# Optimization experiments

Hardware: AMD Instinct MI355X
Metric: run time of the kernel (lower is better)

The kernel has to match this reference:

```python
import jax, jax.numpy as jnp
import numpy as np

A = 20000        # distinct library arcs
T = 500000       # timing arcs in design
S = 8            # LUT slew-axis length
C = 8            # LUT load-axis length
G = 250000       # gates
TOTAL_U = 1000000  # gate x candidate-master entries
SCALE = 1.0e15
MAX_CAP = 1.0e-12
MAX_ITER = 3


def _axis_interval(ax, x):
    """ax: [M,K] monotone axes, x: [M]. Returns lower index i0 in [0,K-2] and frac a (may extrapolate)."""
    K = ax.shape[1]
    i0 = jnp.clip(jnp.sum(ax <= x[:, None], axis=1) - 1, 0, K - 2)
    ar = jnp.arange(ax.shape[0])
    x0 = ax[ar, i0]
    x1 = ax[ar, i0 + 1]
    a = (x - x0) / (x1 - x0)
    return i0, a


def _bilinear_gate(in_slew, load, dtab, stab, axs, axc):
    """Batched bilinear interpolation into per-arc 2D LUTs. All leading dims M."""
    M = in_slew.shape[0]
    ar = jnp.arange(M)
    i0, a = _axis_interval(axs, in_slew)
    j0, b = _axis_interval(axc, load)
    i1, j1 = i0 + 1, j0 + 1

    def _blerp(t):
        return ((1 - a) * (1 - b) * t[ar, i0, j0]
                + (1 - a) * b * t[ar, i0, j1]
                + a * (1 - b) * t[ar, i1, j0]
                + a * b * t[ar, i1, j1])

    return _blerp(dtab), _blerp(stab)


def _compute_ceff_batch(in_slew, c1, c2, rpi, dtab, stab, axs, axc, max_iter=MAX_ITER):
    ceff = jnp.maximum(c1 + c2, 1e-30)
    for _ in range(max_iter):
        d, _ = _bilinear_gate(in_slew, ceff, dtab, stab, axs, axc)
        tau = jnp.maximum(d, 1e-30)
        ratio = jnp.minimum(2.0 * tau / jnp.maximum(in_slew, 1e-30), 10.0)
        h = jnp.where(ratio > 0.01, (1.0 - jnp.exp(-ratio)) / ratio, 1.0 - ratio / 2.0)
        ceff = jnp.maximum(c1 + c2 * h, 1e-30)
    return ceff


def _segment_softmax(logits, gate_id, num_groups):
    """Numerically stable per-gate softmax via segment reductions."""
    gmax = jax.ops.segment_max(logits, gate_id, num_segments=num_groups)
    ex = jnp.exp(logits - gmax[gate_id])
    gsum = jax.ops.segment_sum(ex, gate_id, num_segments=num_groups)
    return ex / gsum[gate_id]


def _gate_grouped_forward(in_arr, in_slew, c1, c2, rpi, arc_idx_r, arc_idx_f,
                          unateness, delay_table, slew_table, load_index, slew_index):
    t = arc_idx_r.shape[0]
    arc_flat = jnp.stack([arc_idx_r, arc_idx_f], axis=1).reshape(-1)  # [2T]
    una = unateness[arc_flat]
    is_fall = jnp.arange(2 * t, dtype=una.dtype) % 2
    rf_idx = (una ^ is_fall).reshape(t, 2)  # rise/fall select per column
    in_slew_sel = jnp.take_along_axis(in_slew, rf_idx, axis=1).reshape(-1)
    in_arr_sel = jnp.take_along_axis(in_arr, rf_idx, axis=1).reshape(-1)

    dtab = delay_table[arc_flat]   # [2T,S,C] big gather (memory bound)
    stab = slew_table[arc_flat]
    axc = load_index[arc_flat]     # [2T,C]
    axs = slew_index[arc_flat]     # [2T,S]

    c1_f = jnp.repeat(c1, 2) / SCALE
    c2_f = jnp.repeat(c2, 2) / SCALE
    rpi_f = jnp.repeat(rpi, 2)
    load = _compute_ceff_batch(in_slew_sel, c1_f, c2_f, rpi_f, dtab, stab, axs, axc)
    load = jnp.minimum(load, MAX_CAP)

    arc_delay, arc_slew = _bilinear_gate(in_slew_sel, load, dtab, stab, axs, axc)
    arr_out = (in_arr_sel + arc_delay).reshape(t, 2)
    slew_out = arc_slew.reshape(t, 2)
    return jnp.concatenate([arr_out, slew_out], axis=1)  # [T,4]


def setup_inputs() -> dict:
    key = jax.random.key(0)
    ks = jax.random.split(key, 14)
    U_flat = jax.random.normal(ks[0], (TOTAL_U,), jnp.float32)
    gate_id = jnp.sort(jax.random.randint(ks[1], (TOTAL_U,), 0, G, dtype=jnp.int32))
    in_arr = jax.random.normal(ks[2], (T, 2), jnp.float32)
    in_slew = jax.random.uniform(ks[3], (T, 2), jnp.float32, 0.05, 3.0)
    c1 = jax.random.uniform(ks[4], (T,), jnp.float32, 0.0, 1.0)
    c2 = jax.random.uniform(ks[5], (T,), jnp.float32, 0.0, 1.0)
    rpi = jax.random.uniform(ks[6], (T,), jnp.float32, 0.1, 1.0)
    arc_idx_r = jax.random.randint(ks[7], (T,), 0, A, dtype=jnp.int32)
    arc_idx_f = jax.random.randint(ks[8], (T,), 0, A, dtype=jnp.int32)
    unateness = jax.random.randint(ks[9], (A,), 0, 2, dtype=jnp.int32)
    delay_table = jax.random.uniform(ks[10], (A, S, C), jnp.float32, 0.01, 1.0)
    slew_table = jax.random.uniform(ks[11], (A, S, C), jnp.float32, 0.01, 1.0)
    # strictly increasing LUT axes: slew axis ~[0.05, 4], load axis ~[5e-17, 3e-15]
    slew_index = jnp.cumsum(jax.random.uniform(ks[12], (A, S), jnp.float32, 0.05, 0.6), axis=1)
    load_index = jnp.cumsum(jax.random.uniform(ks[13], (A, C), jnp.float32, 0.05, 0.6), axis=1) * 1e-15
    return dict(U_flat=U_flat, gate_id=gate_id, in_arr=in_arr, in_slew=in_slew,
                c1=c1, c2=c2, rpi=rpi, arc_idx_r=arc_idx_r, arc_idx_f=arc_idx_f,
                unateness=unateness, delay_table=delay_table, slew_table=slew_table,
                slew_index=slew_index, load_index=load_index)


def reference(U_flat, gate_id, in_arr, in_slew, c1, c2, rpi, arc_idx_r, arc_idx_f,
              unateness, delay_table, slew_table, slew_index, load_index):
    weights = _segment_softmax(U_flat, gate_id, G)  # per-gate soft master selection
    out = _gate_grouped_forward(in_arr, in_slew, c1, c2, rpi, arc_idx_r, arc_idx_f,
                                unateness, delay_table, slew_table, load_index, slew_index)
    return out, weights
```

## Files before the change

kernel.cpp:

```cpp
#include <hip/hip_runtime.h>

#define T_N 500000
#define U_N 1000000
#define A_N 20000

#define SBLK 256
#define HALO 96

#define TIMING_BLOCKS ((T_N + 255) / 256)
#define SOFTMAX_BLOCKS ((U_N + SBLK - 1) / SBLK)

typedef float vfloat2 __attribute__((ext_vector_type(2)));
typedef float vfloat4 __attribute__((ext_vector_type(4)));
typedef float vfloat8 __attribute__((ext_vector_type(8)));

__device__ __forceinline__ float sel8(vfloat8 r, int j) {
    float v = r[0];
    v = (j >= 1) ? r[1] : v;
    v = (j >= 2) ? r[2] : v;
    v = (j >= 3) ? r[3] : v;
    v = (j >= 4) ? r[4] : v;
    v = (j >= 5) ? r[5] : v;
    v = (j >= 6) ? r[6] : v;
    v = (j >= 7) ? r[7] : v;
    return v;
}

__device__ __forceinline__ vfloat8 load8v(const float* __restrict__ p) {
    return *(const vfloat8*)p;
}


__global__ void __launch_bounds__(256, 1)
fused_kernel(
             const float2* __restrict__ in_arr,
             const float2* __restrict__ in_slew,
             const float* __restrict__ c1,
             const float* __restrict__ c2,
             const int* __restrict__ arc_r,
             const int* __restrict__ arc_f,
             const int* __restrict__ una,
             const float* __restrict__ dtab,
             const float* __restrict__ stab,
             const float* __restrict__ sidx,
             const float* __restrict__ lidx,
             float4* __restrict__ out,
             const float* __restrict__ U,
             const int* __restrict__ gid,
             float* __restrict__ wout)
{
    __shared__ float se[SBLK + 2 * HALO];
    __shared__ int   sg[SBLK + 2 * HALO];

    if (blockIdx.x >= TIMING_BLOCKS) {
        int sblk = blockIdx.x - TIMING_BLOCKS;
        int base = sblk * SBLK;
        int wstart = base - HALO;

        for (int k = threadIdx.x; k < SBLK + 2 * HALO; k += SBLK) {
            int idx = wstart + k;
            if (idx >= 0 && idx < U_N) {
                se[k] = expf(__builtin_nontemporal_load(U + idx));
                sg[k] = __builtin_nontemporal_load(gid + idx);
            } else {
                se[k] = 0.0f;
                sg[k] = -1 - k;
            }
        }
        __syncthreads();

        int i = base + threadIdx.x;
        if (i >= U_N) return;

        int li = threadIdx.x + HALO;
        int g = sg[li];
        float mye = se[li];
        float s = mye;
        for (int j = li - 1; j >= 0 && sg[j] == g; --j) s += se[j];
        for (int j = li + 1; j < SBLK + 2 * HALO && sg[j] == g; ++j) s += se[j];

        __builtin_nontemporal_store(mye / s, wout + i);
        return;
    }

    int t = blockIdx.x * blockDim.x + threadIdx.x;
    if (t >= T_N) return;

    vfloat2 ia = __builtin_nontemporal_load((const vfloat2*)in_arr + t);
    vfloat2 is = __builtin_nontemporal_load((const vfloat2*)in_slew + t);
    float c1f = __builtin_nontemporal_load(c1 + t) / 1.0e15f;
    float c2f = __builtin_nontemporal_load(c2 + t) / 1.0e15f;
    int arcs0 = __builtin_nontemporal_load(arc_r + t);
    int arcs1 = __builtin_nontemporal_load(arc_f + t);

    float res_arr[2], res_slew[2];

#pragma unroll
    for (int col = 0; col < 2; ++col) {
        int arc = (col == 0) ? arcs0 : arcs1;
        int u   = una[arc];
        int rf  = u ^ col;
        float slew = rf ? is.y : is.x;
        float arr  = rf ? ia.y : ia.x;

        vfloat8 s  = load8v(sidx + (size_t)arc * 8);
        vfloat8 cx = load8v(lidx + (size_t)arc * 8);

        int cnt = 0;
#pragma unroll
        for (int k = 0; k < 8; ++k) cnt += (s[k] <= slew) ? 1 : 0;
        int i0 = min(max(cnt - 1, 0), 6);
        float x0 = sel8(s, i0);
        float x1 = sel8(s, i0 + 1);
        float a = (slew - x0) / (x1 - x0);
        float om_a = 1.0f - a;

        vfloat8 d0 = load8v(dtab + (size_t)arc * 64 + (size_t)i0 * 8);
        vfloat8 d1 = load8v(dtab + (size_t)arc * 64 + (size_t)i0 * 8 + 8);

        float slew_den = fmaxf(slew, 1e-30f);
        float ceff = fmaxf(c1f + c2f, 1e-30f);
#pragma unroll
        for (int it = 0; it < 3; ++it) {
            int jc = 0;
#pragma unroll
            for (int k = 0; k < 8; ++k) jc += (cx[k] <= ceff) ? 1 : 0;
            int j0 = min(max(jc - 1, 0), 6);
            float y0 = sel8(cx, j0);
            float y1 = sel8(cx, j0 + 1);
            float b = (ceff - y0) / (y1 - y0);
            float om_b = 1.0f - b;
            float v00 = sel8(d0, j0), v01 = sel8(d0, j0 + 1);
            float v10 = sel8(d1, j0), v11 = sel8(d1, j0 + 1);
            float d = om_a * om_b * v00 + om_a * b * v01
                    + a * om_b * v10 + a * b * v11;
            float tau = fmaxf(d, 1e-30f);
            float ratio = fminf(2.0f * tau / slew_den, 10.0f);
            float h = (ratio > 0.01f) ? (1.0f - expf(-ratio)) / ratio
                                      : 1.0f - 0.5f * ratio;
            ceff = fmaxf(c1f + c2f * h, 1e-30f);
        }
        float load = fminf(ceff, 1.0e-12f);

        int jc = 0;
#pragma unroll
        for (int k = 0; k < 8; ++k) jc += (cx[k] <= load) ? 1 : 0;
        int j0 = min(max(jc - 1, 0), 6);
        float y0 = sel8(cx, j0);
        float y1 = sel8(cx, j0 + 1);
        float b = (load - y0) / (y1 - y0);
        float om_b = 1.0f - b;

        float v00 = sel8(d0, j0), v01 = sel8(d0, j0 + 1);
        float v10 = sel8(d1, j0), v11 = sel8(d1, j0 + 1);
        float delay = om_a * om_b * v00 + om_a * b * v01
                    + a * om_b * v10 + a * b * v11;

        const float* srow = stab + (size_t)arc * 64 + (size_t)i0 * 8;
        float s00 = srow[j0],     s01 = srow[j0 + 1];
        float s10 = srow[8 + j0], s11 = srow[8 + j0 + 1];
        float sl = om_a * om_b * s00 + om_a * b * s01
                 + a * om_b * s10 + a * b * s11;

        res_arr[col]  = arr + delay;
        res_slew[col] = sl;
    }

    vfloat4 o = {res_arr[0], res_arr[1], res_slew[0], res_slew[1]};
    __builtin_nontemporal_store(o, (vfloat4*)out + t);
}

extern "C" void kernel_launch(void* const* d_in, const int* in_sizes, int n_in,
                              void* d_out, int out_size, void* d_ws, size_t ws_size,
                              hipStream_t stream) {
    const float*  U      = (const float*)d_in[0];
    const int*    gid    = (const int*)d_in[1];
    const float2* in_arr = (const float2*)d_in[2];
    const float2* in_slw = (const float2*)d_in[3];
    const float*  c1     = (const float*)d_in[4];
    const float*  c2     = (const float*)d_in[5];
    const int*    arc_r  = (const int*)d_in[7];
    const int*    arc_f  = (const int*)d_in[8];
    const int*    una    = (const int*)d_in[9];
    const float*  dtab   = (const float*)d_in[10];
    const float*  stab   = (const float*)d_in[11];
    const float*  sidx   = (const float*)d_in[12];
    const float*  lidx   = (const float*)d_in[13];

    float* out  = (float*)d_out;
    float* wout = out + (size_t)T_N * 4;

    fused_kernel<<<TIMING_BLOCKS + SOFTMAX_BLOCKS, 256, 0, stream>>>(
        in_arr, in_slw, c1, c2, arc_r, arc_f, una, dtab, stab, sidx, lidx,
        (float4*)out, U, gid, wout);
}
```

Baseline: 144.9 us.

## Repack LUT axes and tables into interleaved workspace layout, bit-pack unateness into LDS

A pre-pass kernel interleaves the slew and load axes per arc, interleaves the delay and slew tables row by row, and packs unateness into a bitmask. The main kernel loads that bitmask into shared memory per timing block and reads the interleaved layouts, so each random arc gather touches fewer cache lines. The cost is an extra launch plus about 11 MB of repacking traffic on every call, and a per-block LDS fill of 625 words. A fallback path keeps the original kernel when the workspace is too small.

```diff
diff --git a/kernel.cpp b/kernel.cpp
--- a/kernel.cpp
+++ b/kernel.cpp
@@ -9,6 +9,13 @@
 
 #define TIMING_BLOCKS ((T_N + 255) / 256)
 #define SOFTMAX_BLOCKS ((U_N + SBLK - 1) / SBLK)
+
+#define UNA_WORDS ((A_N + 31) / 32)
+#define META_BYTES (A_N * 16 * 4)
+#define UNA_BYTES  (UNA_WORDS * 4)
+#define PK_BYTES   (A_N * 128 * 4)
+#define WS_META    (META_BYTES + UNA_BYTES)
+#define WS_FULL    (META_BYTES + UNA_BYTES + PK_BYTES)
 
 typedef float vfloat2 __attribute__((ext_vector_type(2)));
 typedef float vfloat4 __attribute__((ext_vector_type(4)));
@@ -31,26 +38,60 @@
 }
 
 
+__global__ void __launch_bounds__(256)
+repack_kernel(const float* __restrict__ sidx, const float* __restrict__ lidx,
+              const float* __restrict__ dtab, const float* __restrict__ stab,
+              const int* __restrict__ una,
+              float* __restrict__ meta, unsigned* __restrict__ una_pk,
+              float* __restrict__ pk, int do_tables)
+{
+    int gtid = blockIdx.x * 256 + threadIdx.x;
+    int gs   = gridDim.x * 256;
+    for (int i = gtid; i < A_N * 8; i += gs) {
+        int a = i >> 3, k = i & 7;
+        meta[(size_t)a * 16 + k]     = __builtin_nontemporal_load(sidx + i);
+        meta[(size_t)a * 16 + 8 + k] = __builtin_nontemporal_load(lidx + i);
+    }
+    for (int w = gtid; w < UNA_WORDS; w += gs) {
+        unsigned bits = 0;
+        int base = w * 32;
+        int lim = min(32, A_N - base);
+        for (int b = 0; b < lim; ++b)
+            bits |= (unsigned)(una[base + b] & 1) << b;
+        una_pk[w] = bits;
+    }
+    if (do_tables) {
+        for (int i = gtid; i < A_N * 64; i += gs) {
+            int a = i >> 6, kj = i & 63;
+            int k = kj >> 3, j = kj & 7;
+            size_t b = (size_t)a * 128 + (size_t)k * 16 + j;
+            pk[b]     = __builtin_nontemporal_load(dtab + i);
+            pk[b + 8] = __builtin_nontemporal_load(stab + i);
+        }
+    }
+}
+
 __global__ void __launch_bounds__(256, 1)
-fused_kernel(
-             const float2* __restrict__ in_arr,
+fused_kernel(const float2* __restrict__ in_arr,
              const float2* __restrict__ in_slew,
              const float* __restrict__ c1,
              const float* __restrict__ c2,
              const int* __restrict__ arc_r,
              const int* __restrict__ arc_f,
-             const int* __restrict__ una,
              const float* __restrict__ dtab,
              const float* __restrict__ stab,
-             const float* __restrict__ sidx,
-             const float* __restrict__ lidx,
+             const float* __restrict__ meta,
+             const unsigned* __restrict__ una_pk,
+             const float* __restrict__ pk,
+             int use_pk,
              float4* __restrict__ out,
              const float* __restrict__ U,
              const int* __restrict__ gid,
              float* __restrict__ wout)
 {
-    __shared__ float se[SBLK + 2 * HALO];
-    __shared__ int   sg[SBLK + 2 * HALO];
+    __shared__ float    se[SBLK + 2 * HALO];
+    __shared__ int      sg[SBLK + 2 * HALO];
+    __shared__ unsigned una_lds[UNA_WORDS];
 
     if (blockIdx.x >= TIMING_BLOCKS) {
         int sblk = blockIdx.x - TIMING_BLOCKS;
@@ -83,6 +124,10 @@
         return;
     }
 
+    for (int k = threadIdx.x; k < UNA_WORDS; k += 256)
+        una_lds[k] = una_pk[k];
+    __syncthreads();
+
     int t = blockIdx.x * blockDim.x + threadIdx.x;
     if (t >= T_N) return;
 
@@ -98,25 +143,33 @@
 #pragma unroll
     for (int col = 0; col < 2; ++col) {
         int arc = (col == 0) ? arcs0 : arcs1;
-        int u   = una[arc];
+        int u   = (una_lds[arc >> 5] >> (arc & 31)) & 1;
         int rf  = u ^ col;
         float slew = rf ? is.y : is.x;
         float arr  = rf ? ia.y : ia.x;
 
-        vfloat8 s  = load8v(sidx + (size_t)arc * 8);
-        vfloat8 cx = load8v(lidx + (size_t)arc * 8);
+        const float* mrow = meta + (size_t)arc * 16;
+        vfloat8 sx = load8v(mrow);
+        vfloat8 cx = load8v(mrow + 8);
 
         int cnt = 0;
 #pragma unroll
-        for (int k = 0; k < 8; ++k) cnt += (s[k] <= slew) ? 1 : 0;
+        for (int k = 0; k < 8; ++k) cnt += (sx[k] <= slew) ? 1 : 0;
         int i0 = min(max(cnt - 1, 0), 6);
-        float x0 = sel8(s, i0);
-        float x1 = sel8(s, i0 + 1);
+        float x0 = sel8(sx, i0);
+        float x1 = sel8(sx, i0 + 1);
         float a = (slew - x0) / (x1 - x0);
         float om_a = 1.0f - a;
 
-        vfloat8 d0 = load8v(dtab + (size_t)arc * 64 + (size_t)i0 * 8);
-        vfloat8 d1 = load8v(dtab + (size_t)arc * 64 + (size_t)i0 * 8 + 8);
+        vfloat8 d0, d1;
+        const float* prow = pk + (size_t)arc * 128 + (size_t)i0 * 16;
+        if (use_pk) {
+            d0 = load8v(prow);
+            d1 = load8v(prow + 16);
+        } else {
+            d0 = load8v(dtab + (size_t)arc * 64 + (size_t)i0 * 8);
+            d1 = load8v(dtab + (size_t)arc * 64 + (size_t)i0 * 8 + 8);
+        }
 
         float slew_den = fmaxf(slew, 1e-30f);
         float ceff = fmaxf(c1f + c2f, 1e-30f);
@@ -156,16 +209,137 @@
         float delay = om_a * om_b * v00 + om_a * b * v01
                     + a * om_b * v10 + a * b * v11;
 
+        float s00, s01, s10, s11;
+        if (use_pk) {
+            vfloat8 e0 = load8v(prow + 8);
+            vfloat8 e1 = load8v(prow + 24);
+            s00 = sel8(e0, j0); s01 = sel8(e0, j0 + 1);
+            s10 = sel8(e1, j0); s11 = sel8(e1, j0 + 1);
+        } else {
+            const float* srow = stab + (size_t)arc * 64 + (size_t)i0 * 8;
+            s00 = srow[j0];     s01 = srow[j0 + 1];
+            s10 = srow[8 + j0]; s11 = srow[8 + j0 + 1];
+        }
+        float sl = om_a * om_b * s00 + om_a * b * s01
+                 + a * om_b * s10 + a * b * s11;
+
+        res_arr[col]  = arr + delay;
+        res_slew[col] = sl;
+    }
+
+    vfloat4 o = {res_arr[0], res_arr[1], res_slew[0], res_slew[1]};
+    __builtin_nontemporal_store(o, (vfloat4*)out + t);
+}
+
+__global__ void __launch_bounds__(256, 1)
+fused_fb(const float2* __restrict__ in_arr, const float2* __restrict__ in_slew,
+         const float* __restrict__ c1, const float* __restrict__ c2,
+         const int* __restrict__ arc_r, const int* __restrict__ arc_f,
+         const int* __restrict__ una,
+         const float* __restrict__ dtab, const float* __restrict__ stab,
+         const float* __restrict__ sidx, const float* __restrict__ lidx,
+         float4* __restrict__ out,
+         const float* __restrict__ U, const int* __restrict__ gid,
+         float* __restrict__ wout)
+{
+    __shared__ float se[SBLK + 2 * HALO];
+    __shared__ int   sg[SBLK + 2 * HALO];
+
+    if (blockIdx.x >= TIMING_BLOCKS) {
+        int sblk = blockIdx.x - TIMING_BLOCKS;
+        int base = sblk * SBLK;
+        int wstart = base - HALO;
+        for (int k = threadIdx.x; k < SBLK + 2 * HALO; k += SBLK) {
+            int idx = wstart + k;
+            if (idx >= 0 && idx < U_N) {
+                se[k] = expf(__builtin_nontemporal_load(U + idx));
+                sg[k] = __builtin_nontemporal_load(gid + idx);
+            } else { se[k] = 0.0f; sg[k] = -1 - k; }
+        }
+        __syncthreads();
+        int i = base + threadIdx.x;
+        if (i >= U_N) return;
+        int li = threadIdx.x + HALO;
+        int g = sg[li];
+        float mye = se[li];
+        float s = mye;
+        for (int j = li - 1; j >= 0 && sg[j] == g; --j) s += se[j];
+        for (int j = li + 1; j < SBLK + 2 * HALO && sg[j] == g; ++j) s += se[j];
+        __builtin_nontemporal_store(mye / s, wout + i);
+        return;
+    }
+
+    int t = blockIdx.x * blockDim.x + threadIdx.x;
+    if (t >= T_N) return;
+    vfloat2 ia = __builtin_nontemporal_load((const vfloat2*)in_arr + t);
+    vfloat2 is = __builtin_nontemporal_load((const vfloat2*)in_slew + t);
+    float c1f = __builtin_nontemporal_load(c1 + t) / 1.0e15f;
+    float c2f = __builtin_nontemporal_load(c2 + t) / 1.0e15f;
+    int arcs0 = __builtin_nontemporal_load(arc_r + t);
+    int arcs1 = __builtin_nontemporal_load(arc_f + t);
+    float res_arr[2], res_slew[2];
+#pragma unroll
+    for (int col = 0; col < 2; ++col) {
+        int arc = (col == 0) ? arcs0 : arcs1;
+        int u   = una[arc];
+        int rf  = u ^ col;
+        float slew = rf ? is.y : is.x;
+        float arr  = rf ? ia.y : ia.x;
+        vfloat8 s  = load8v(sidx + (size_t)arc * 8);
+        vfloat8 cx = load8v(lidx + (size_t)arc * 8);
+        int cnt = 0;
+#pragma unroll
+        for (int k = 0; k < 8; ++k) cnt += (s[k] <= slew) ? 1 : 0;
+        int i0 = min(max(cnt - 1, 0), 6);
+        float x0 = sel8(s, i0);
+        float x1 = sel8(s, i0 + 1);
+        float a = (slew - x0) / (x1 - x0);
+        float om_a = 1.0f - a;
+        vfloat8 d0 = load8v(dtab + (size_t)arc * 64 + (size_t)i0 * 8);
+        vfloat8 d1 = load8v(dtab + (size_t)arc * 64 + (size_t)i0 * 8 + 8);
+        float slew_den = fmaxf(slew, 1e-30f);
+        float ceff = fmaxf(c1f + c2f, 1e-30f);
+#pragma unroll
+        for (int it = 0; it < 3; ++it) {
+            int jc = 0;
+#pragma unroll
+            for (int k = 0; k < 8; ++k) jc += (cx[k] <= ceff) ? 1 : 0;
+            int j0 = min(max(jc - 1, 0), 6);
+            float y0 = sel8(cx, j0);
+            float y1 = sel8(cx, j0 + 1);
+            float b = (ceff - y0) / (y1 - y0);
+            float om_b = 1.0f - b;
+            float v00 = sel8(d0, j0), v01 = sel8(d0, j0 + 1);
+            float v10 = sel8(d1, j0), v11 = sel8(d1, j0 + 1);
+            float d = om_a * om_b * v00 + om_a * b * v01
+                    + a * om_b * v10 + a * b * v11;
+            float tau = fmaxf(d, 1e-30f);
+            float ratio = fminf(2.0f * tau / slew_den, 10.0f);
+            float h = (ratio > 0.01f) ? (1.0f - expf(-ratio)) / ratio
+                                      : 1.0f - 0.5f * ratio;
+            ceff = fmaxf(c1f + c2f * h, 1e-30f);
+        }
+        float load = fminf(ceff, 1.0e-12f);
+        int jc = 0;
+#pragma unroll
+        for (int k = 0; k < 8; ++k) jc += (cx[k] <= load) ? 1 : 0;
+        int j0 = min(max(jc - 1, 0), 6);
+        float y0 = sel8(cx, j0);
+        float y1 = sel8(cx, j0 + 1);
+        float b = (load - y0) / (y1 - y0);
+        float om_b = 1.0f - b;
+        float v00 = sel8(d0, j0), v01 = sel8(d0, j0 + 1);
+        float v10 = sel8(d1, j0), v11 = sel8(d1, j0 + 1);
+        float delay = om_a * om_b * v00 + om_a * b * v01
+                    + a * om_b * v10 + a * b * v11;
         const float* srow = stab + (size_t)arc * 64 + (size_t)i0 * 8;
         float s00 = srow[j0],     s01 = srow[j0 + 1];
         float s10 = srow[8 + j0], s11 = srow[8 + j0 + 1];
         float sl = om_a * om_b * s00 + om_a * b * s01
                  + a * om_b * s10 + a * b * s11;
-
         res_arr[col]  = arr + delay;
         res_slew[col] = sl;
     }
-
     vfloat4 o = {res_arr[0], res_arr[1], res_slew[0], res_slew[1]};
     __builtin_nontemporal_store(o, (vfloat4*)out + t);
 }
@@ -190,7 +364,22 @@
     float* out  = (float*)d_out;
     float* wout = out + (size_t)T_N * 4;
 
-    fused_kernel<<<TIMING_BLOCKS + SOFTMAX_BLOCKS, 256, 0, stream>>>(
-        in_arr, in_slw, c1, c2, arc_r, arc_f, una, dtab, stab, sidx, lidx,
-        (float4*)out, U, gid, wout);
-}
+    bool meta_ok = (d_ws != nullptr) && (ws_size >= (size_t)WS_META);
+    bool full    = (d_ws != nullptr) && (ws_size >= (size_t)WS_FULL);
+
+    if (meta_ok) {
+        float*    meta   = (float*)d_ws;
+        unsigned* una_pk = (unsigned*)((char*)d_ws + META_BYTES);
+        float*    pk     = (float*)((char*)d_ws + META_BYTES + UNA_BYTES);
+
+        repack_kernel<<<512, 256, 0, stream>>>(sidx, lidx, dtab, stab, una,
+                                               meta, una_pk, pk, full ? 1 : 0);
+        fused_kernel<<<TIMING_BLOCKS + SOFTMAX_BLOCKS, 256, 0, stream>>>(
+            in_arr, in_slw, c1, c2, arc_r, arc_f, dtab, stab,
+            meta, una_pk, pk, full ? 1 : 0, (float4*)out, U, gid, wout);
+    } else {
+        fused_fb<<<TIMING_BLOCKS + SOFTMAX_BLOCKS, 256, 0, stream>>>(
+            in_arr, in_slw, c1, c2, arc_r, arc_f, una, dtab, stab, sidx, lidx,
+            (float4*)out, U, gid, wout);
+    }
+}
```

Result: slower. 158.7 us (+9.5%).
